# Kernel optimization log

Measured on AMD Instinct MI355X. Metric: run time of the kernel, lower is better.

The kernel has to match this reference:

```python
import jax, jax.numpy as jnp
import numpy as np

B, S, D, H = 32, 64, 256, 8
HD = D // H
NS = S + 1
TH = 0.5
LN_EPS = 1e-5


def _lin(k, out_d, in_d, gain=1.0):
    lim = gain * np.sqrt(6.0 / (in_d + out_d))
    return jax.random.uniform(k, (out_d, in_d), minval=-lim, maxval=lim, dtype=jnp.float32)


def setup_inputs() -> dict:
    key = jax.random.key(0)
    ks = jax.random.split(key, 16)
    g = 1.0 / np.sqrt(2.0)
    return {
        'desc_embeddings': jax.random.normal(ks[0], (B, S, D), dtype=jnp.float32),
        'name_value_embeddings': jax.random.normal(ks[1], (B, NS, D), dtype=jnp.float32),
        'Wg': _lin(ks[2], D, D), 'bg': jnp.zeros((D,), jnp.float32),
        'Wq': _lin(ks[3], D, D, g), 'bq': jnp.zeros((D,), jnp.float32),
        'Wk': _lin(ks[4], D, D, g), 'bk': jnp.zeros((D,), jnp.float32),
        'Wv': _lin(ks[5], D, D, g), 'bv': jnp.zeros((D,), jnp.float32),
        'We1': _lin(ks[6], D, 2 * D), 'be1': jnp.zeros((D,), jnp.float32),
        'lng': jnp.ones((D,), jnp.float32), 'lnb': jnp.zeros((D,), jnp.float32),
        'We2': _lin(ks[7], D, D), 'be2': jnp.zeros((D,), jnp.float32),
        'Wa': _lin(ks[8], 1, 3 * HD, g), 'ba': jnp.zeros((1,), jnp.float32),
        'Wo': _lin(ks[9], D, D, g), 'bo': jnp.zeros((D,), jnp.float32),
        'tb': jnp.zeros((1,), jnp.float32),
    }


def reference(desc_embeddings, name_value_embeddings, Wg, bg, Wq, bq, Wk, bk, Wv, bv,
              We1, be1, lng, lnb, We2, be2, Wa, ba, Wo, bo, tb):
    # 1. Global topology
    desc = desc_embeddings @ Wg.T + bg                      # [B,S,D]
    dn = desc / jnp.linalg.norm(desc, axis=-1, keepdims=True)
    gsim = jnp.einsum('bid,bjd->bij', dn, dn)
    gt = jax.nn.sigmoid(gsim + tb[0])
    # straight-through threshold
    A = (gt > TH).astype(gt.dtype) - jax.lax.stop_gradient(gt) + gt
    # 2. Sample-wise similarity
    var = name_value_embeddings[:, 1:, :]
    vn = var / jnp.linalg.norm(var, axis=-1, keepdims=True)
    ssim = jnp.einsum('bid,bjd->bij', vn, vn)
    A = A * (1.0 - jnp.eye(S, dtype=A.dtype))               # no self-interaction
    adjacency = jax.nn.softmax(A * ssim, axis=-1)
    # 4. Edge attrs & adjacency (scatter-assembled, CLS at index 0)
    var_edge = jnp.concatenate([
        jnp.broadcast_to(desc[:, :, None, :], (B, S, S, D)),
        jnp.broadcast_to(desc[:, None, :, :], (B, S, S, D))], axis=-1)  # [B,S,S,2D]
    cls_edge = jnp.concatenate([desc, desc], axis=-1)       # [B,S,2D]
    ea = jnp.zeros((B, NS, NS, 2 * D), jnp.float32)
    ea = ea.at[:, 1:, 1:].set(var_edge).at[:, 0, 1:].set(cls_edge).at[:, 1:, 0].set(cls_edge)
    na = jnp.zeros((B, NS, NS), jnp.float32)
    na = na.at[:, 1:, 1:].set(adjacency).at[:, 0, 1:].set(1.0)
    # 5. Attention
    q = (name_value_embeddings @ Wq.T + bq).reshape(B, NS, H, HD).transpose(0, 2, 1, 3)
    k = (name_value_embeddings @ Wk.T + bk).reshape(B, NS, H, HD).transpose(0, 2, 1, 3)
    v = (name_value_embeddings @ Wv.T + bv).reshape(B, NS, H, HD).transpose(0, 2, 1, 3)
    h = ea @ We1.T + be1
    mu = h.mean(axis=-1, keepdims=True)
    sig = ((h - mu) ** 2).mean(axis=-1, keepdims=True)
    h = (h - mu) / jnp.sqrt(sig + LN_EPS) * lng + lnb
    e = jax.nn.relu(h) @ We2.T + be2                        # [B,NS,NS,D]
    e = e.reshape(B, NS, NS, H, HD).transpose(0, 3, 1, 2, 4)  # [B,H,NS,NS,HD]
    e = e * na[:, None, :, :, None]
    # attn_proj(concat(q_i, k_j, e_ij)) decomposed into three dot products
    wq, wk_, we = Wa[0, :HD], Wa[0, HD:2 * HD], Wa[0, 2 * HD:]
    sq = jnp.einsum('bhid,d->bhi', q, wq)
    sk = jnp.einsum('bhjd,d->bhj', k, wk_)
    se = jnp.einsum('bhijd,d->bhij', e, we)
    scores = sq[:, :, :, None] + sk[:, :, None, :] + se + ba[0]
    scores = scores + (na[:, None, :, :] == 0).astype(scores.dtype) * -1e9
    aw = jax.nn.softmax(scores, axis=-1)                    # [B,H,NS,NS]
    ctx = jnp.einsum('bhij,bhjd->bhid', aw, v).transpose(0, 2, 1, 3).reshape(B, NS, D)
    out = ctx @ Wo.T + bo
    return (out, aw)
```

## Files before the change

kernel.cpp:

```cpp
#include <hip/hip_runtime.h>
#include <hip/hip_bf16.h>

#define BB 32
#define SS 64
#define DD 256
#define HH 8
#define HDIM 32
#define NSS 65
#define LN_EPS 1e-5f

#define OFF_DESC   0u
#define OFF_DESCT  524288u
#define OFF_U      1048576u
#define OFF_VT     1572864u
#define OFF_VART   2097152u
#define OFF_VBUF   2621440u
#define OFF_SQ     3153920u
#define OFF_SK     3170560u
#define OFF_CTX    3187200u
#define OFF_WGT    3719680u
#define OFF_WE1AT  3785216u
#define OFF_WE1BT  3850752u
#define OFF_WVT    3916288u
#define OFF_WOT    3981824u
#define OFF_CUT    4047360u
#define OFF_CVT    4112896u
#define OFF_BU     4178432u
#define OFF_BV     4178688u
#define OFF_WQF    4178944u
#define OFF_WKF    4180992u
#define OFF_CVEC   4183040u
#define OFF_RND    4183072u
#define OFF_RNV    4185120u
#define OFF_PKG    4187168u
#define OFF_PKM    4187680u

__device__ __forceinline__ void gemm16_body(const float* __restrict__ in,
                                            const float* __restrict__ WT,
                                            const float* __restrict__ bias,
                                            float* __restrict__ out,
                                            float* __restrict__ outT,
                                            int r0, int addBias, float* vals) {
    int o = threadIdx.x;
    const float* __restrict__ x = in + (size_t)r0 * DD;
    float acc[16];
    #pragma unroll
    for (int r = 0; r < 16; ++r) acc[r] = 0.f;
    #pragma unroll 4
    for (int k = 0; k < DD; ++k) {
        float w = WT[(size_t)k * DD + o];
        #pragma unroll
        for (int r = 0; r < 16; ++r)
            acc[r] = fmaf(x[r * DD + k], w, acc[r]);
    }
    float bb = addBias ? bias[o] : 0.f;
    #pragma unroll
    for (int r = 0; r < 16; ++r) vals[r] = acc[r] + bb;
    if (out) {
        #pragma unroll
        for (int r = 0; r < 16; ++r)
            out[(size_t)(r0 + r) * DD + o] = vals[r];
    }
    if (outT) {
        size_t base = (size_t)(r0 >> 6) * 16384 + (size_t)(o >> 2) * 256 + (o & 3);
        int j0 = r0 & 63;
        #pragma unroll
        for (int r = 0; r < 16; ++r)
            outT[base + (size_t)(j0 + r) * 4] = vals[r];
    }
}

__global__ __launch_bounds__(256) void prep_a(
    const float* __restrict__ Wg, const float* __restrict__ We1,
    const float* __restrict__ Wv, const float* __restrict__ Wo,
    const float* __restrict__ Wq, const float* __restrict__ bq,
    const float* __restrict__ Wk, const float* __restrict__ bk,
    const float* __restrict__ We2, const float* __restrict__ be2,
    const float* __restrict__ Wa, const float* __restrict__ lng,
    const float* __restrict__ lnb,
    float* __restrict__ WgT, float* __restrict__ We1aT, float* __restrict__ We1bT,
    float* __restrict__ WvT, float* __restrict__ WoT,
    float* __restrict__ wqf, float* __restrict__ wkf,
    float* __restrict__ PKg, float* __restrict__ PKm, float* __restrict__ cvec) {
    __shared__ float t[64][65];
    int blk = blockIdx.x;
    if (blk < 80) {
        int which = blk >> 4, t16 = blk & 15;
        const float* src; float* dst; int ld, c0;
        if (which == 0)      { src = Wg;  dst = WgT;   ld = 256; c0 = 0; }
        else if (which == 1) { src = We1; dst = We1aT; ld = 512; c0 = 0; }
        else if (which == 2) { src = We1; dst = We1bT; ld = 512; c0 = 256; }
        else if (which == 3) { src = Wv;  dst = WvT;   ld = 256; c0 = 0; }
        else                 { src = Wo;  dst = WoT;   ld = 256; c0 = 0; }
        int to = t16 & 3, tk = t16 >> 2;
        int tx = threadIdx.x & 63, ty = threadIdx.x >> 6;
        #pragma unroll
        for (int r = ty; r < 64; r += 4)
            t[r][tx] = src[(size_t)(to * 64 + r) * ld + c0 + tk * 64 + tx];
        __syncthreads();
        #pragma unroll
        for (int r = ty; r < 64; r += 4)
            dst[(size_t)(tk * 64 + r) * DD + to * 64 + tx] = t[tx][r];
    } else if (blk < 88) {
        int h = blk - 80, in = threadIdx.x;
        float aq = 0.f, ak = 0.f, ae = 0.f;
        #pragma unroll
        for (int d = 0; d < HDIM; ++d) {
            aq = fmaf(Wq[(h * HDIM + d) * DD + in], Wa[d], aq);
            ak = fmaf(Wk[(h * HDIM + d) * DD + in], Wa[HDIM + d], ak);
            ae = fmaf(We2[(h * HDIM + d) * DD + in], Wa[2 * HDIM + d], ae);
        }
        wqf[h * DD + in] = aq;
        wkf[h * DD + in] = ak;
        PKm[in * HH + h] = ae;
        if (in == 0) {
            float cq = 0.f, ck = 0.f, ce = 0.f;
            for (int d = 0; d < HDIM; ++d) {
                cq = fmaf(bq[h * HDIM + d], Wa[d], cq);
                ck = fmaf(bk[h * HDIM + d], Wa[HDIM + d], ck);
                ce = fmaf(be2[h * HDIM + d], Wa[2 * HDIM + d], ce);
            }
            cvec[h] = cq; cvec[8 + h] = ck; cvec[16 + h] = ce;
        }
    } else {
        int d = threadIdx.x;
        PKg[d * 2] = lng[d];
        PKg[d * 2 + 1] = lnb[d];
    }
}

__global__ __launch_bounds__(256) void prep_b(
    const float* __restrict__ WgT, const float* __restrict__ We1aT,
    const float* __restrict__ We1bT, const float* __restrict__ bg,
    const float* __restrict__ be1,
    float* __restrict__ CuT, float* __restrict__ CvT,
    float* __restrict__ bu, float* __restrict__ bv) {
    float vals[16];
    int blk = blockIdx.x;
    if (blk < 16) gemm16_body(WgT, We1aT, nullptr, CuT, nullptr, blk * 16, 0, vals);
    else if (blk < 32) gemm16_body(WgT, We1bT, nullptr, CvT, nullptr, (blk - 16) * 16, 0, vals);
    else if (blk == 32) {
        int o = threadIdx.x;
        float a = be1[o];
        for (int m = 0; m < DD; ++m) a = fmaf(We1aT[(size_t)m * DD + o], bg[m], a);
        bu[o] = a;
    } else {
        int o = threadIdx.x;
        float a = 0.f;
        for (int m = 0; m < DD; ++m) a = fmaf(We1bT[(size_t)m * DD + o], bg[m], a);
        bv[o] = a;
    }
}

__global__ __launch_bounds__(256) void proj_kernel(
    const float* __restrict__ X, const float* __restrict__ nve,
    const float* __restrict__ WgT, const float* __restrict__ CuT,
    const float* __restrict__ CvT, const float* __restrict__ WvT,
    const float* __restrict__ bg, const float* __restrict__ bu,
    const float* __restrict__ bv, const float* __restrict__ bwv,
    const float* __restrict__ wqf, const float* __restrict__ wkf,
    const float* __restrict__ cvec,
    float* __restrict__ desc, float* __restrict__ descT,
    float* __restrict__ U, float* __restrict__ VT,
    float* __restrict__ varT, float* __restrict__ vbuf,
    float* __restrict__ sq, float* __restrict__ sk,
    float* __restrict__ rnd, float* __restrict__ rnv) {
    __shared__ float red[4][16];
    float vals[16];
    int blk = blockIdx.x;
    if (blk < 128) {
        gemm16_body(X, WgT, bg, desc, descT, blk * 16, 1, vals);
        int w = threadIdx.x >> 6, lane = threadIdx.x & 63;
        #pragma unroll
        for (int r = 0; r < 16; ++r) {
            float s2 = vals[r] * vals[r];
            #pragma unroll
            for (int off = 32; off; off >>= 1) s2 += __shfl_xor(s2, off);
            if (lane == 0) red[w][r] = s2;
        }
        __syncthreads();
        if (threadIdx.x < 16) {
            float s = red[0][threadIdx.x] + red[1][threadIdx.x] +
                      red[2][threadIdx.x] + red[3][threadIdx.x];
            rnd[blk * 16 + threadIdx.x] = 1.f / sqrtf(s);
        }
    } else if (blk < 256) {
        gemm16_body(X, CuT, bu, U, nullptr, (blk - 128) * 16, 1, vals);
    } else if (blk < 384) {
        gemm16_body(X, CvT, bv, nullptr, VT, (blk - 256) * 16, 1, vals);
    } else if (blk < 514) {
        gemm16_body(nve, WvT, bwv, vbuf, nullptr, (blk - 384) * 16, 1, vals);
    } else if (blk < 644) {
        int r0 = (blk - 514) * 16;
        int lr = threadIdx.x >> 4, tq = threadIdx.x & 15;
        int g = r0 + lr, b = g / NSS, ii = g % NSS;
        const float* __restrict__ x = nve + (size_t)g * DD;
        const float* __restrict__ wv = ((tq < 8) ? wqf : wkf) + (tq & 7) * DD;
        float acc = 0.f;
        #pragma unroll 8
        for (int k = 0; k < DD; ++k) acc = fmaf(x[k], wv[k], acc);
        int h = tq & 7;
        if (tq < 8) sq[(size_t)(b * HH + h) * NSS + ii] = acc + cvec[h];
        else        sk[(size_t)(b * HH + h) * NSS + ii] = acc + cvec[8 + h];
    } else if (blk < 772) {
        int r0 = (blk - 644) * 16;
        int lr = threadIdx.x >> 4, tq = threadIdx.x & 15;
        int g = r0 + lr, b = g >> 6, s = g & 63;
        const float* __restrict__ x = nve + (size_t)(b * NSS + 1 + s) * DD;
        float ssum = 0.f;
        for (int k = tq; k < DD; k += 16) ssum = fmaf(x[k], x[k], ssum);
        ssum += __shfl_xor(ssum, 1);
        ssum += __shfl_xor(ssum, 2);
        ssum += __shfl_xor(ssum, 4);
        ssum += __shfl_xor(ssum, 8);
        if (tq == 0) rnv[g] = 1.f / sqrtf(ssum);
    } else {
        int b = blk - 772;
        int d = threadIdx.x;
        size_t base = (size_t)b * 16384 + (size_t)(d >> 2) * 256 + (d & 3);
        const float* __restrict__ src = nve + ((size_t)b * NSS + 1) * DD + d;
        #pragma unroll 4
        for (int j = 0; j < 64; ++j)
            varT[base + (size_t)j * 4] = src[(size_t)j * DD];
    }
}

__global__ __launch_bounds__(256) void se_attn_kernel(
    const float* __restrict__ desc, const float* __restrict__ descT,
    const float* __restrict__ nve,  const float* __restrict__ varT,
    const float* __restrict__ U,    const float* __restrict__ VT,
    const float* __restrict__ vbuf,
    const float* __restrict__ rnd,  const float* __restrict__ rnv,
    const float* __restrict__ sq,   const float* __restrict__ sk,
    const float* __restrict__ PKg,  const float* __restrict__ PKm,
    const float* __restrict__ cvec, const float* __restrict__ ba,
    const float* __restrict__ tb,
    float* __restrict__ aw, float* __restrict__ ctx) {
    __shared__ float SH[4224];
    int t = blockIdx.x >> 5, b = blockIdx.x & 31;
    int w = threadIdx.x >> 6, lane = threadIdx.x & 63;
    float bav = ba[0];

    if (t < 16) {
        int iu = __builtin_amdgcn_readfirstlane(t * 4 + w);
        int i = iu + 1;
        const float4* __restrict__ dT4  = (const float4*)(descT + (size_t)b * 16384);
        const float4* __restrict__ vrT4 = (const float4*)(varT  + (size_t)b * 16384);
        const float4* __restrict__ vt4  = (const float4*)(VT    + (size_t)b * 16384);
        const float4* __restrict__ di4 = (const float4*)(desc + (size_t)(b * SS + iu) * DD);
        const float4* __restrict__ vi4 = (const float4*)(nve + (size_t)(b * NSS + 1 + iu) * DD);
        const float4* __restrict__ ui4 = (const float4*)(U + (size_t)(b * SS + iu) * DD);

        float gd0 = 0.f, gd1 = 0.f, vd0 = 0.f, vd1 = 0.f;
        #pragma unroll 8
        for (int f = 0; f < 64; ++f) {
            float4 a = dT4[f * 64 + lane];  float4 u1 = di4[f];
            float4 c = vrT4[f * 64 + lane]; float4 u2 = vi4[f];
            gd0 = fmaf(a.x, u1.x, gd0); gd1 = fmaf(a.y, u1.y, gd1);
            gd0 = fmaf(a.z, u1.z, gd0); gd1 = fmaf(a.w, u1.w, gd1);
            vd0 = fmaf(c.x, u2.x, vd0); vd1 = fmaf(c.y, u2.y, vd1);
            vd0 = fmaf(c.z, u2.z, vd0); vd1 = fmaf(c.w, u2.w, vd1);
        }
        float gsim = (gd0 + gd1) * rnd[b * SS + iu] * rnd[b * SS + lane];
        float ssim = (vd0 + vd1) * rnv[b * SS + iu] * rnv[b * SS + lane];
        bool flag = (gsim + tb[0] > 0.f) && (iu != lane);
        float P = flag ? ssim : 0.f;
        float e = __expf(P);
        float s = e;
        #pragma unroll
        for (int off = 32; off; off >>= 1) s += __shfl_xor(s, off);
        float nav = e / s;

        float ssum = 0.f, s2 = 0.f;
        #pragma unroll 8
        for (int f = 0; f < 64; ++f) {
            float4 v = vt4[f * 64 + lane]; float4 u = ui4[f];
            float t0 = v.x + u.x, t1 = v.y + u.y, t2 = v.z + u.z, t3 = v.w + u.w;
            ssum += (t0 + t1) + (t2 + t3);
            s2 = fmaf(t0, t0, s2); s2 = fmaf(t1, t1, s2);
            s2 = fmaf(t2, t2, s2); s2 = fmaf(t3, t3, s2);
        }
        float mu = ssum * (1.f / DD);
        float var = fmaf(-mu, mu, s2 * (1.f / DD));
        float rstd = rsqrtf(var + LN_EPS);

        float p[HH];
        #pragma unroll
        for (int h = 0; h < HH; ++h) p[h] = 0.f;
        #pragma unroll 2
        for (int f = 0; f < 64; ++f) {
            float4 v = vt4[f * 64 + lane]; float4 u = ui4[f];
            const float4* __restrict__ pg = (const float4*)(PKg + 8 * f);
            float4 pg0 = pg[0], pg1 = pg[1];
            float tv[4] = {v.x + u.x, v.y + u.y, v.z + u.z, v.w + u.w};
            float gv[4] = {pg0.x, pg0.z, pg1.x, pg1.z};
            float bv_[4] = {pg0.y, pg0.w, pg1.y, pg1.w};
            #pragma unroll
            for (int c = 0; c < 4; ++c) {
                const float4* __restrict__ m4 = (const float4*)(PKm + (size_t)(4 * f + c) * HH);
                float4 mlo = m4[0], mhi = m4[1];
                float xn = fmaf((tv[c] - mu) * rstd, gv[c], bv_[c]);
                float r = fmaxf(xn, 0.f);
                p[0] = fmaf(r, mlo.x, p[0]); p[1] = fmaf(r, mlo.y, p[1]);
                p[2] = fmaf(r, mlo.z, p[2]); p[3] = fmaf(r, mlo.w, p[3]);
                p[4] = fmaf(r, mhi.x, p[4]); p[5] = fmaf(r, mhi.y, p[5]);
                p[6] = fmaf(r, mhi.z, p[6]); p[7] = fmaf(r, mhi.w, p[7]);
            }
        }

        float* awL = SH + w * 528;
        #pragma unroll
        for (int h = 0; h < HH; ++h) {
            float sev = nav * (p[h] + cvec[16 + h]);
            float sc = sq[(size_t)(b * HH + h) * NSS + i] +
                       sk[(size_t)(b * HH + h) * NSS + 1 + lane] + sev + bav;
            float m = sc;
            #pragma unroll
            for (int off = 32; off; off >>= 1) m = fmaxf(m, __shfl_xor(m, off));
            float e2 = __expf(sc - m);
            float tot = e2;
            #pragma unroll
            for (int off = 32; off; off >>= 1) tot += __shfl_xor(tot, off);
            float aval = e2 / tot;
            float* awrow = aw + ((size_t)(b * HH + h) * NSS + i) * NSS;
            awrow[1 + lane] = aval;
            if (lane == 0) awrow[0] = 0.f;
            awL[h * 66 + lane] = aval;
        }
        const float* __restrict__ awh = awL + (lane >> 3) * 66;
        const float4* __restrict__ vb4 = (const float4*)(vbuf + ((size_t)b * NSS + 1) * DD);
        float cx = 0.f, cy = 0.f, cz = 0.f, cw = 0.f;
        #pragma unroll 4
        for (int j = 0; j < 64; ++j) {
            float a = awh[j];
            float4 v = vb4[(size_t)j * 64 + lane];
            cx = fmaf(a, v.x, cx); cy = fmaf(a, v.y, cy);
            cz = fmaf(a, v.z, cz); cw = fmaf(a, v.w, cw);
        }
        *(float4*)(ctx + ((size_t)(b * NSS) + i) * DD + 4 * lane) =
            make_float4(cx, cy, cz, cw);
    } else {
        float* tile = SH;
        int dloc = lane & 31, jh = lane >> 5;
        float ss = 0.f, s2 = 0.f;
        for (int c = 0; c < 4; ++c) {
            for (int jr = w; jr < 64; jr += 4)
                tile[jr * 65 + lane] = U[(size_t)(b * SS + jr) * DD + c * 64 + lane];
            __syncthreads();
            #pragma unroll 8
            for (int dd = 0; dd < 64; ++dd) {
                int d = c * 64 + dd;
                float u = tile[lane * 65 + dd];
                float v = VT[(size_t)b * 16384 + (size_t)(d >> 2) * 256 + lane * 4 + (d & 3)];
                float t2 = u + v; ss += t2; s2 = fmaf(t2, t2, s2);
            }
            __syncthreads();
        }
        float mu = ss * (1.f / DD);
        float va = fmaf(-mu, mu, s2 * (1.f / DD));
        float rstd = rsqrtf(va + LN_EPS);
        float p[HH];
        #pragma unroll
        for (int h = 0; h < HH; ++h) p[h] = 0.f;
        for (int c = 0; c < 4; ++c) {
            for (int jr = w; jr < 64; jr += 4)
                tile[jr * 65 + lane] = U[(size_t)(b * SS + jr) * DD + c * 64 + lane];
            __syncthreads();
            #pragma unroll 4
            for (int dd = 0; dd < 64; ++dd) {
                int d = c * 64 + dd;
                float u = tile[lane * 65 + dd];
                float v = VT[(size_t)b * 16384 + (size_t)(d >> 2) * 256 + lane * 4 + (d & 3)];
                float t2 = u + v;
                float rv = fmaxf(fmaf((t2 - mu) * rstd, PKg[d * 2], PKg[d * 2 + 1]), 0.f);
                const float* __restrict__ m8 = PKm + (size_t)d * HH;
                #pragma unroll
                for (int h = 0; h < HH; ++h) p[h] = fmaf(rv, m8[h], p[h]);
            }
            __syncthreads();
        }
        float sel0 = 0.f, sel1 = 0.f;
        #pragma unroll
        for (int h = 0; h < HH; ++h) {
            if (h == w * 2)     sel0 = p[h];
            if (h == w * 2 + 1) sel1 = p[h];
        }
        #pragma unroll
        for (int q = 0; q < 2; ++q) {
            int h = w * 2 + q;
            float dot = q ? sel1 : sel0;
            float sev = dot + cvec[16 + h];
            float skh = sk[(size_t)(b * HH + h) * NSS + 1 + lane];
            float sc = sq[(size_t)(b * HH + h) * NSS] + skh + sev + bav;
            float m = sc;
            #pragma unroll
            for (int off = 32; off; off >>= 1) m = fmaxf(m, __shfl_xor(m, off));
            float e = __expf(sc - m), s = e;
            #pragma unroll
            for (int off = 32; off; off >>= 1) s += __shfl_xor(s, off);
            float aval = e / s;
            float* awrow = aw + ((size_t)(b * HH + h) * NSS) * NSS;
            awrow[1 + lane] = aval;
            if (lane == 0) awrow[0] = 0.f;
            float acc = 0.f;
            #pragma unroll
            for (int j2 = 0; j2 < 32; ++j2) {
                int jj = j2 * 2 + jh;
                float a = __shfl(aval, jj);
                acc = fmaf(a, vbuf[((size_t)(b * NSS) + 1 + jj) * DD + h * HDIM + dloc], acc);
            }
            acc += __shfl_xor(acc, 32);
            if (lane < 32)
                ctx[(size_t)(b * NSS) * DD + h * HDIM + dloc] = acc;
        }
    }
}

__global__ __launch_bounds__(256) void outgemm_kernel(
    const float* __restrict__ ctx, const float* __restrict__ WoT,
    const float* __restrict__ bo, float* __restrict__ out) {
    float vals[16];
    gemm16_body(ctx, WoT, bo, out, nullptr, blockIdx.x * 16, 1, vals);
}

extern "C" void kernel_launch(void* const* d_in, const int* in_sizes, int n_in,
                              void* d_out, int out_size, void* d_ws, size_t ws_size,
                              hipStream_t stream) {
    const float* desc_emb = (const float*)d_in[0];
    const float* nve      = (const float*)d_in[1];
    const float* Wg  = (const float*)d_in[2];
    const float* bg  = (const float*)d_in[3];
    const float* Wq  = (const float*)d_in[4];
    const float* bq  = (const float*)d_in[5];
    const float* Wk  = (const float*)d_in[6];
    const float* bk  = (const float*)d_in[7];
    const float* Wv  = (const float*)d_in[8];
    const float* bv_in = (const float*)d_in[9];
    const float* We1 = (const float*)d_in[10];
    const float* be1 = (const float*)d_in[11];
    const float* lng = (const float*)d_in[12];
    const float* lnb = (const float*)d_in[13];
    const float* We2 = (const float*)d_in[14];
    const float* be2 = (const float*)d_in[15];
    const float* Wa  = (const float*)d_in[16];
    const float* ba  = (const float*)d_in[17];
    const float* Wo  = (const float*)d_in[18];
    const float* bo  = (const float*)d_in[19];
    const float* tb  = (const float*)d_in[20];

    float* ws    = (float*)d_ws;
    float* desc  = ws + OFF_DESC;
    float* descT = ws + OFF_DESCT;
    float* U     = ws + OFF_U;
    float* VT    = ws + OFF_VT;
    float* varT  = ws + OFF_VART;
    float* vbuf  = ws + OFF_VBUF;
    float* sq    = ws + OFF_SQ;
    float* sk    = ws + OFF_SK;
    float* ctx   = ws + OFF_CTX;
    float* WgT   = ws + OFF_WGT;
    float* We1aT = ws + OFF_WE1AT;
    float* We1bT = ws + OFF_WE1BT;
    float* WvT   = ws + OFF_WVT;
    float* WoT   = ws + OFF_WOT;
    float* CuT   = ws + OFF_CUT;
    float* CvT   = ws + OFF_CVT;
    float* bu    = ws + OFF_BU;
    float* bv    = ws + OFF_BV;
    float* wqf   = ws + OFF_WQF;
    float* wkf   = ws + OFF_WKF;
    float* cvec  = ws + OFF_CVEC;
    float* rnd   = ws + OFF_RND;
    float* rnv   = ws + OFF_RNV;
    float* PKg   = ws + OFF_PKG;
    float* PKm   = ws + OFF_PKM;

    float* out = (float*)d_out;
    float* aw  = out + (size_t)BB * NSS * DD;

    prep_a<<<89, 256, 0, stream>>>(Wg, We1, Wv, Wo, Wq, bq, Wk, bk, We2, be2,
                                   Wa, lng, lnb,
                                   WgT, We1aT, We1bT, WvT, WoT,
                                   wqf, wkf, PKg, PKm, cvec);
    prep_b<<<34, 256, 0, stream>>>(WgT, We1aT, We1bT, bg, be1, CuT, CvT, bu, bv);
    proj_kernel<<<804, 256, 0, stream>>>(desc_emb, nve, WgT, CuT, CvT, WvT,
                                         bg, bu, bv, bv_in, wqf, wkf, cvec,
                                         desc, descT, U, VT, varT, vbuf,
                                         sq, sk, rnd, rnv);
    se_attn_kernel<<<544, 256, 0, stream>>>(desc, descT, nve, varT, U, VT,
                                            vbuf, rnd, rnv, sq, sk,
                                            PKg, PKm, cvec, ba, tb, aw, ctx);
    outgemm_kernel<<<130, 256, 0, stream>>>(ctx, WoT, bo, out);
}
```

Before: 156.9 us.

## Split each attention row across two waves over feature halves

The per-row attention blocks now give each query row to a pair of waves. Each wave handles half of the feature dimension, and the partial dot products, LayerNorm statistics and head projections are combined through shared memory. The grid grows from 544 to 1056 blocks, which shortens each wave's serial loop and raises parallelism. The separate statistics pass is fused into the similarity loop. In exchange it adds block-wide barriers and shared-memory reductions, and the context accumulation uses a split-j scheme with a cross-lane shuffle.

Result: slower. 222.1 us (+41.6%).

```diff
diff --git a/kernel.cpp b/kernel.cpp
--- a/kernel.cpp
+++ b/kernel.cpp
@@ -237,13 +237,16 @@
     const float* __restrict__ tb,
     float* __restrict__ aw, float* __restrict__ ctx) {
     __shared__ float SH[4224];
-    int t = blockIdx.x >> 5, b = blockIdx.x & 31;
+    int bid = blockIdx.x;
     int w = threadIdx.x >> 6, lane = threadIdx.x & 63;
     float bav = ba[0];
 
-    if (t < 16) {
-        int iu = __builtin_amdgcn_readfirstlane(t * 4 + w);
+    if (bid < 1024) {
+        int t = bid >> 5, b = bid & 31;
+        int z = w >> 1, q = w & 1;
+        int iu = __builtin_amdgcn_readfirstlane(t * 2 + z);
         int i = iu + 1;
+        int f0 = q * 32;
         const float4* __restrict__ dT4  = (const float4*)(descT + (size_t)b * 16384);
         const float4* __restrict__ vrT4 = (const float4*)(varT  + (size_t)b * 16384);
         const float4* __restrict__ vt4  = (const float4*)(VT    + (size_t)b * 16384);
@@ -251,18 +254,31 @@
         const float4* __restrict__ vi4 = (const float4*)(nve + (size_t)(b * NSS + 1 + iu) * DD);
         const float4* __restrict__ ui4 = (const float4*)(U + (size_t)(b * SS + iu) * DD);
 
-        float gd0 = 0.f, gd1 = 0.f, vd0 = 0.f, vd1 = 0.f;
-        #pragma unroll 8
-        for (int f = 0; f < 64; ++f) {
-            float4 a = dT4[f * 64 + lane];  float4 u1 = di4[f];
-            float4 c = vrT4[f * 64 + lane]; float4 u2 = vi4[f];
-            gd0 = fmaf(a.x, u1.x, gd0); gd1 = fmaf(a.y, u1.y, gd1);
-            gd0 = fmaf(a.z, u1.z, gd0); gd1 = fmaf(a.w, u1.w, gd1);
-            vd0 = fmaf(c.x, u2.x, vd0); vd1 = fmaf(c.y, u2.y, vd1);
-            vd0 = fmaf(c.z, u2.z, vd0); vd1 = fmaf(c.w, u2.w, vd1);
-        }
-        float gsim = (gd0 + gd1) * rnd[b * SS + iu] * rnd[b * SS + lane];
-        float ssim = (vd0 + vd1) * rnv[b * SS + iu] * rnv[b * SS + lane];
+        float gd = 0.f, vd = 0.f, ssum = 0.f, s2 = 0.f;
+        #pragma unroll 4
+        for (int f = 0; f < 32; ++f) {
+            int ff = f0 + f;
+            float4 a = dT4[ff * 64 + lane];  float4 u1 = di4[ff];
+            float4 c = vrT4[ff * 64 + lane]; float4 u2 = vi4[ff];
+            float4 v = vt4[ff * 64 + lane];  float4 u = ui4[ff];
+            gd = fmaf(a.x, u1.x, gd); gd = fmaf(a.y, u1.y, gd);
+            gd = fmaf(a.z, u1.z, gd); gd = fmaf(a.w, u1.w, gd);
+            vd = fmaf(c.x, u2.x, vd); vd = fmaf(c.y, u2.y, vd);
+            vd = fmaf(c.z, u2.z, vd); vd = fmaf(c.w, u2.w, vd);
+            float t0 = v.x + u.x, t1 = v.y + u.y, t2 = v.z + u.z, t3 = v.w + u.w;
+            ssum += (t0 + t1) + (t2 + t3);
+            s2 = fmaf(t0, t0, s2); s2 = fmaf(t1, t1, s2);
+            s2 = fmaf(t2, t2, s2); s2 = fmaf(t3, t3, s2);
+        }
+        float4* statL = (float4*)SH;
+        statL[w * 64 + lane] = make_float4(gd, vd, ssum, s2);
+        __syncthreads();
+        float4 o = statL[(w ^ 1) * 64 + lane];
+        float mu = (ssum + o.z) * (1.f / DD);
+        float var = fmaf(-mu, mu, (s2 + o.w) * (1.f / DD));
+        float rstd = rsqrtf(var + LN_EPS);
+        float gsim = (gd + o.x) * rnd[b * SS + iu] * rnd[b * SS + lane];
+        float ssim = (vd + o.y) * rnv[b * SS + iu] * rnv[b * SS + lane];
         bool flag = (gsim + tb[0] > 0.f) && (iu != lane);
         float P = flag ? ssim : 0.f;
         float e = __expf(P);
@@ -271,35 +287,23 @@
         for (int off = 32; off; off >>= 1) s += __shfl_xor(s, off);
         float nav = e / s;
 
-        float ssum = 0.f, s2 = 0.f;
-        #pragma unroll 8
-        for (int f = 0; f < 64; ++f) {
-            float4 v = vt4[f * 64 + lane]; float4 u = ui4[f];
-            float t0 = v.x + u.x, t1 = v.y + u.y, t2 = v.z + u.z, t3 = v.w + u.w;
-            ssum += (t0 + t1) + (t2 + t3);
-            s2 = fmaf(t0, t0, s2); s2 = fmaf(t1, t1, s2);
-            s2 = fmaf(t2, t2, s2); s2 = fmaf(t3, t3, s2);
-        }
-        float mu = ssum * (1.f / DD);
-        float var = fmaf(-mu, mu, s2 * (1.f / DD));
-        float rstd = rsqrtf(var + LN_EPS);
-
         float p[HH];
         #pragma unroll
         for (int h = 0; h < HH; ++h) p[h] = 0.f;
         #pragma unroll 2
-        for (int f = 0; f < 64; ++f) {
-            float4 v = vt4[f * 64 + lane]; float4 u = ui4[f];
-            const float4* __restrict__ pg = (const float4*)(PKg + 8 * f);
+        for (int f = 0; f < 32; ++f) {
+            int ff = f0 + f;
+            float4 v = vt4[ff * 64 + lane]; float4 u = ui4[ff];
+            const float4* __restrict__ pg = (const float4*)(PKg + 8 * ff);
             float4 pg0 = pg[0], pg1 = pg[1];
             float tv[4] = {v.x + u.x, v.y + u.y, v.z + u.z, v.w + u.w};
             float gv[4] = {pg0.x, pg0.z, pg1.x, pg1.z};
             float bv_[4] = {pg0.y, pg0.w, pg1.y, pg1.w};
             #pragma unroll
-            for (int c = 0; c < 4; ++c) {
-                const float4* __restrict__ m4 = (const float4*)(PKm + (size_t)(4 * f + c) * HH);
+            for (int c2 = 0; c2 < 4; ++c2) {
+                const float4* __restrict__ m4 = (const float4*)(PKm + (size_t)(4 * ff + c2) * HH);
                 float4 mlo = m4[0], mhi = m4[1];
-                float xn = fmaf((tv[c] - mu) * rstd, gv[c], bv_[c]);
+                float xn = fmaf((tv[c2] - mu) * rstd, gv[c2], bv_[c2]);
                 float r = fmaxf(xn, 0.f);
                 p[0] = fmaf(r, mlo.x, p[0]); p[1] = fmaf(r, mlo.y, p[1]);
                 p[2] = fmaf(r, mlo.z, p[2]); p[3] = fmaf(r, mlo.w, p[3]);
@@ -307,11 +311,21 @@
                 p[6] = fmaf(r, mhi.z, p[6]); p[7] = fmaf(r, mhi.w, p[7]);
             }
         }
-
-        float* awL = SH + w * 528;
-        #pragma unroll
-        for (int h = 0; h < HH; ++h) {
-            float sev = nav * (p[h] + cvec[16 + h]);
+        float* sepL = SH + 1024;
+        #pragma unroll
+        for (int h = 0; h < HH; ++h) sepL[w * 512 + h * 64 + lane] = p[h];
+        __syncthreads();
+        #pragma unroll
+        for (int h = 0; h < HH; ++h) p[h] += sepL[(w ^ 1) * 512 + h * 64 + lane];
+        float psel[4];
+        #pragma unroll
+        for (int hh = 0; hh < 4; ++hh) psel[hh] = q ? p[4 + hh] : p[hh];
+
+        float* awL = SH + 3072 + z * 528;
+        #pragma unroll
+        for (int hh = 0; hh < 4; ++hh) {
+            int h = q * 4 + hh;
+            float sev = nav * (psel[hh] + cvec[16 + h]);
             float sc = sq[(size_t)(b * HH + h) * NSS + i] +
                        sk[(size_t)(b * HH + h) * NSS + 1 + lane] + sev + bav;
             float m = sc;
@@ -327,19 +341,29 @@
             if (lane == 0) awrow[0] = 0.f;
             awL[h * 66 + lane] = aval;
         }
-        const float* __restrict__ awh = awL + (lane >> 3) * 66;
+        __syncthreads();
+
+        int qd = q * 32 + (lane & 31);
+        int head = qd >> 3;
+        int jh = lane >> 5;
+        const float* __restrict__ awh = SH + 3072 + z * 528 + head * 66;
         const float4* __restrict__ vb4 = (const float4*)(vbuf + ((size_t)b * NSS + 1) * DD);
         float cx = 0.f, cy = 0.f, cz = 0.f, cw = 0.f;
-        #pragma unroll 4
-        for (int j = 0; j < 64; ++j) {
+        #pragma unroll 8
+        for (int j2 = 0; j2 < 32; ++j2) {
+            int j = j2 * 2 + jh;
             float a = awh[j];
-            float4 v = vb4[(size_t)j * 64 + lane];
+            float4 v = vb4[(size_t)j * 64 + qd];
             cx = fmaf(a, v.x, cx); cy = fmaf(a, v.y, cy);
             cz = fmaf(a, v.z, cz); cw = fmaf(a, v.w, cw);
         }
-        *(float4*)(ctx + ((size_t)(b * NSS) + i) * DD + 4 * lane) =
-            make_float4(cx, cy, cz, cw);
+        cx += __shfl_xor(cx, 32); cy += __shfl_xor(cy, 32);
+        cz += __shfl_xor(cz, 32); cw += __shfl_xor(cw, 32);
+        if (lane < 32)
+            *(float4*)(ctx + ((size_t)(b * NSS) + i) * DD + qd * 4) =
+                make_float4(cx, cy, cz, cw);
     } else {
+        int b = bid - 1024;
         float* tile = SH;
         int dloc = lane & 31, jh = lane >> 5;
         float ss = 0.f, s2 = 0.f;
@@ -386,9 +410,9 @@
             if (h == w * 2 + 1) sel1 = p[h];
         }
         #pragma unroll
-        for (int q = 0; q < 2; ++q) {
-            int h = w * 2 + q;
-            float dot = q ? sel1 : sel0;
+        for (int q2 = 0; q2 < 2; ++q2) {
+            int h = w * 2 + q2;
+            float dot = q2 ? sel1 : sel0;
             float sev = dot + cvec[16 + h];
             float skh = sk[(size_t)(b * HH + h) * NSS + 1 + lane];
             float sc = sq[(size_t)(b * HH + h) * NSS] + skh + sev + bav;
@@ -487,8 +511,8 @@
                                          bg, bu, bv, bv_in, wqf, wkf, cvec,
                                          desc, descT, U, VT, varT, vbuf,
                                          sq, sk, rnd, rnv);
-    se_attn_kernel<<<544, 256, 0, stream>>>(desc, descT, nve, varT, U, VT,
-                                            vbuf, rnd, rnv, sq, sk,
-                                            PKg, PKm, cvec, ba, tb, aw, ctx);
+    se_attn_kernel<<<1056, 256, 0, stream>>>(desc, descT, nve, varT, U, VT,
+                                             vbuf, rnd, rnv, sq, sk,
+                                             PKg, PKm, cvec, ba, tb, aw, ctx);
     outgemm_kernel<<<130, 256, 0, stream>>>(ctx, WoT, bo, out);
 }
```

## Halve GEMM rows per block and fuse LayerNorm stats into similarity loop

Applied to the files above, without the earlier changes.

The 16-row GEMM helper becomes a template on row count. The projection and output GEMMs now use 8 rows per block, which doubles their grid sizes and gives more blocks across the CUs. In the edge-attention kernel, the separate loop that computed LayerNorm sum and sum-of-squares over U+VT is merged into the loop that computes the gsim/ssim dot products, so the per-row inputs are streamed once instead of twice. In exchange, each GEMM block reuses each weight load across fewer rows, the fused loop puts more register pressure on the kernel, and the single accumulator chains add latency.

Result: faster. 146.2 us, median of 2 (-6.8%).

```diff
diff --git a/kernel.cpp b/kernel.cpp
--- a/kernel.cpp
+++ b/kernel.cpp
@@ -35,37 +35,38 @@
 #define OFF_PKG    4187168u
 #define OFF_PKM    4187680u
 
-__device__ __forceinline__ void gemm16_body(const float* __restrict__ in,
-                                            const float* __restrict__ WT,
-                                            const float* __restrict__ bias,
-                                            float* __restrict__ out,
-                                            float* __restrict__ outT,
-                                            int r0, int addBias, float* vals) {
+template <int R>
+__device__ __forceinline__ void gemmR_body(const float* __restrict__ in,
+                                           const float* __restrict__ WT,
+                                           const float* __restrict__ bias,
+                                           float* __restrict__ out,
+                                           float* __restrict__ outT,
+                                           int r0, int addBias, float* vals) {
     int o = threadIdx.x;
     const float* __restrict__ x = in + (size_t)r0 * DD;
-    float acc[16];
+    float acc[R];
     #pragma unroll
-    for (int r = 0; r < 16; ++r) acc[r] = 0.f;
+    for (int r = 0; r < R; ++r) acc[r] = 0.f;
     #pragma unroll 4
     for (int k = 0; k < DD; ++k) {
         float w = WT[(size_t)k * DD + o];
         #pragma unroll
-        for (int r = 0; r < 16; ++r)
+        for (int r = 0; r < R; ++r)
             acc[r] = fmaf(x[r * DD + k], w, acc[r]);
     }
     float bb = addBias ? bias[o] : 0.f;
     #pragma unroll
-    for (int r = 0; r < 16; ++r) vals[r] = acc[r] + bb;
+    for (int r = 0; r < R; ++r) vals[r] = acc[r] + bb;
     if (out) {
         #pragma unroll
-        for (int r = 0; r < 16; ++r)
+        for (int r = 0; r < R; ++r)
             out[(size_t)(r0 + r) * DD + o] = vals[r];
     }
     if (outT) {
         size_t base = (size_t)(r0 >> 6) * 16384 + (size_t)(o >> 2) * 256 + (o & 3);
         int j0 = r0 & 63;
         #pragma unroll
-        for (int r = 0; r < 16; ++r)
+        for (int r = 0; r < R; ++r)
             outT[base + (size_t)(j0 + r) * 4] = vals[r];
     }
 }
@@ -137,8 +138,8 @@
     float* __restrict__ bu, float* __restrict__ bv) {
     float vals[16];
     int blk = blockIdx.x;
-    if (blk < 16) gemm16_body(WgT, We1aT, nullptr, CuT, nullptr, blk * 16, 0, vals);
-    else if (blk < 32) gemm16_body(WgT, We1bT, nullptr, CvT, nullptr, (blk - 16) * 16, 0, vals);
+    if (blk < 16) gemmR_body<16>(WgT, We1aT, nullptr, CuT, nullptr, blk * 16, 0, vals);
+    else if (blk < 32) gemmR_body<16>(WgT, We1bT, nullptr, CvT, nullptr, (blk - 16) * 16, 0, vals);
     else if (blk == 32) {
         int o = threadIdx.x;
         float a = be1[o];
@@ -165,33 +166,33 @@
     float* __restrict__ varT, float* __restrict__ vbuf,
     float* __restrict__ sq, float* __restrict__ sk,
     float* __restrict__ rnd, float* __restrict__ rnv) {
-    __shared__ float red[4][16];
-    float vals[16];
+    __shared__ float red[4][8];
+    float vals[8];
     int blk = blockIdx.x;
-    if (blk < 128) {
-        gemm16_body(X, WgT, bg, desc, descT, blk * 16, 1, vals);
+    if (blk < 256) {
+        gemmR_body<8>(X, WgT, bg, desc, descT, blk * 8, 1, vals);
         int w = threadIdx.x >> 6, lane = threadIdx.x & 63;
         #pragma unroll
-        for (int r = 0; r < 16; ++r) {
+        for (int r = 0; r < 8; ++r) {
             float s2 = vals[r] * vals[r];
             #pragma unroll
             for (int off = 32; off; off >>= 1) s2 += __shfl_xor(s2, off);
             if (lane == 0) red[w][r] = s2;
         }
         __syncthreads();
-        if (threadIdx.x < 16) {
+        if (threadIdx.x < 8) {
             float s = red[0][threadIdx.x] + red[1][threadIdx.x] +
                       red[2][threadIdx.x] + red[3][threadIdx.x];
-            rnd[blk * 16 + threadIdx.x] = 1.f / sqrtf(s);
-        }
-    } else if (blk < 256) {
-        gemm16_body(X, CuT, bu, U, nullptr, (blk - 128) * 16, 1, vals);
-    } else if (blk < 384) {
-        gemm16_body(X, CvT, bv, nullptr, VT, (blk - 256) * 16, 1, vals);
-    } else if (blk < 514) {
-        gemm16_body(nve, WvT, bwv, vbuf, nullptr, (blk - 384) * 16, 1, vals);
-    } else if (blk < 644) {
-        int r0 = (blk - 514) * 16;
+            rnd[blk * 8 + threadIdx.x] = 1.f / sqrtf(s);
+        }
+    } else if (blk < 512) {
+        gemmR_body<8>(X, CuT, bu, U, nullptr, (blk - 256) * 8, 1, vals);
+    } else if (blk < 768) {
+        gemmR_body<8>(X, CvT, bv, nullptr, VT, (blk - 512) * 8, 1, vals);
+    } else if (blk < 1028) {
+        gemmR_body<8>(nve, WvT, bwv, vbuf, nullptr, (blk - 768) * 8, 1, vals);
+    } else if (blk < 1158) {
+        int r0 = (blk - 1028) * 16;
         int lr = threadIdx.x >> 4, tq = threadIdx.x & 15;
         int g = r0 + lr, b = g / NSS, ii = g % NSS;
         const float* __restrict__ x = nve + (size_t)g * DD;
@@ -202,8 +203,8 @@
         int h = tq & 7;
         if (tq < 8) sq[(size_t)(b * HH + h) * NSS + ii] = acc + cvec[h];
         else        sk[(size_t)(b * HH + h) * NSS + ii] = acc + cvec[8 + h];
-    } else if (blk < 772) {
-        int r0 = (blk - 644) * 16;
+    } else if (blk < 1286) {
+        int r0 = (blk - 1158) * 16;
         int lr = threadIdx.x >> 4, tq = threadIdx.x & 15;
         int g = r0 + lr, b = g >> 6, s = g & 63;
         const float* __restrict__ x = nve + (size_t)(b * NSS + 1 + s) * DD;
@@ -215,7 +216,7 @@
         ssum += __shfl_xor(ssum, 8);
         if (tq == 0) rnv[g] = 1.f / sqrtf(ssum);
     } else {
-        int b = blk - 772;
+        int b = blk - 1286;
         int d = threadIdx.x;
         size_t base = (size_t)b * 16384 + (size_t)(d >> 2) * 256 + (d & 3);
         const float* __restrict__ src = nve + ((size_t)b * NSS + 1) * DD + d;
@@ -251,18 +252,23 @@
         const float4* __restrict__ vi4 = (const float4*)(nve + (size_t)(b * NSS + 1 + iu) * DD);
         const float4* __restrict__ ui4 = (const float4*)(U + (size_t)(b * SS + iu) * DD);
 
-        float gd0 = 0.f, gd1 = 0.f, vd0 = 0.f, vd1 = 0.f;
-        #pragma unroll 8
+        float gd = 0.f, vd = 0.f, ssum = 0.f, s2 = 0.f;
+        #pragma unroll 4
         for (int f = 0; f < 64; ++f) {
             float4 a = dT4[f * 64 + lane];  float4 u1 = di4[f];
             float4 c = vrT4[f * 64 + lane]; float4 u2 = vi4[f];
-            gd0 = fmaf(a.x, u1.x, gd0); gd1 = fmaf(a.y, u1.y, gd1);
-            gd0 = fmaf(a.z, u1.z, gd0); gd1 = fmaf(a.w, u1.w, gd1);
-            vd0 = fmaf(c.x, u2.x, vd0); vd1 = fmaf(c.y, u2.y, vd1);
-            vd0 = fmaf(c.z, u2.z, vd0); vd1 = fmaf(c.w, u2.w, vd1);
-        }
-        float gsim = (gd0 + gd1) * rnd[b * SS + iu] * rnd[b * SS + lane];
-        float ssim = (vd0 + vd1) * rnv[b * SS + iu] * rnv[b * SS + lane];
+            float4 v = vt4[f * 64 + lane];  float4 u = ui4[f];
+            gd = fmaf(a.x, u1.x, gd); gd = fmaf(a.y, u1.y, gd);
+            gd = fmaf(a.z, u1.z, gd); gd = fmaf(a.w, u1.w, gd);
+            vd = fmaf(c.x, u2.x, vd); vd = fmaf(c.y, u2.y, vd);
+            vd = fmaf(c.z, u2.z, vd); vd = fmaf(c.w, u2.w, vd);
+            float t0 = v.x + u.x, t1 = v.y + u.y, t2 = v.z + u.z, t3 = v.w + u.w;
+            ssum += (t0 + t1) + (t2 + t3);
+            s2 = fmaf(t0, t0, s2); s2 = fmaf(t1, t1, s2);
+            s2 = fmaf(t2, t2, s2); s2 = fmaf(t3, t3, s2);
+        }
+        float gsim = gd * rnd[b * SS + iu] * rnd[b * SS + lane];
+        float ssim = vd * rnv[b * SS + iu] * rnv[b * SS + lane];
         bool flag = (gsim + tb[0] > 0.f) && (iu != lane);
         float P = flag ? ssim : 0.f;
         float e = __expf(P);
@@ -270,16 +276,6 @@
         #pragma unroll
         for (int off = 32; off; off >>= 1) s += __shfl_xor(s, off);
         float nav = e / s;
-
-        float ssum = 0.f, s2 = 0.f;
-        #pragma unroll 8
-        for (int f = 0; f < 64; ++f) {
-            float4 v = vt4[f * 64 + lane]; float4 u = ui4[f];
-            float t0 = v.x + u.x, t1 = v.y + u.y, t2 = v.z + u.z, t3 = v.w + u.w;
-            ssum += (t0 + t1) + (t2 + t3);
-            s2 = fmaf(t0, t0, s2); s2 = fmaf(t1, t1, s2);
-            s2 = fmaf(t2, t2, s2); s2 = fmaf(t3, t3, s2);
-        }
         float mu = ssum * (1.f / DD);
         float var = fmaf(-mu, mu, s2 * (1.f / DD));
         float rstd = rsqrtf(var + LN_EPS);
@@ -419,8 +415,8 @@
 __global__ __launch_bounds__(256) void outgemm_kernel(
     const float* __restrict__ ctx, const float* __restrict__ WoT,
     const float* __restrict__ bo, float* __restrict__ out) {
-    float vals[16];
-    gemm16_body(ctx, WoT, bo, out, nullptr, blockIdx.x * 16, 1, vals);
+    float vals[8];
+    gemmR_body<8>(ctx, WoT, bo, out, nullptr, blockIdx.x * 8, 1, vals);
 }
 
 extern "C" void kernel_launch(void* const* d_in, const int* in_sizes, int n_in,
@@ -483,12 +479,12 @@
                                    WgT, We1aT, We1bT, WvT, WoT,
                                    wqf, wkf, PKg, PKm, cvec);
     prep_b<<<34, 256, 0, stream>>>(WgT, We1aT, We1bT, bg, be1, CuT, CvT, bu, bv);
-    proj_kernel<<<804, 256, 0, stream>>>(desc_emb, nve, WgT, CuT, CvT, WvT,
-                                         bg, bu, bv, bv_in, wqf, wkf, cvec,
-                                         desc, descT, U, VT, varT, vbuf,
-                                         sq, sk, rnd, rnv);
+    proj_kernel<<<1318, 256, 0, stream>>>(desc_emb, nve, WgT, CuT, CvT, WvT,
+                                          bg, bu, bv, bv_in, wqf, wkf, cvec,
+                                          desc, descT, U, VT, varT, vbuf,
+                                          sq, sk, rnd, rnv);
     se_attn_kernel<<<544, 256, 0, stream>>>(desc, descT, nve, varT, U, VT,
                                             vbuf, rnd, rnv, sq, sk,
                                             PKg, PKm, cvec, ba, tb, aw, ctx);
-    outgemm_kernel<<<130, 256, 0, stream>>>(ctx, WoT, bo, out);
-}
+    outgemm_kernel<<<260, 256, 0, stream>>>(ctx, WoT, bo, out);
+}
```
